# Kernel optimization log

Measured on AMD Instinct MI355X. Metric: run time of the kernel, lower is better.

Reference implementation:

```python
import jax, jax.numpy as jnp
import numpy as np


def _floor_alpha(q, size):
    # tfa interpolate_bilinear clamps floor to [0, size-2] and alpha to [0, 1]
    floor = jnp.clip(jnp.floor(q), 0.0, float(size - 2))
    alpha = jnp.clip(q - floor, 0.0, 1.0)
    return floor.astype(jnp.int32), alpha


def setup_inputs() -> dict:
    key = jax.random.key(0)
    k1, k2 = jax.random.split(key)
    B, H, W, C = 4, 512, 512, 64
    x = jax.random.normal(k1, (B, H, W, C), dtype=jnp.float32)
    flow = jax.random.normal(k2, (B, H, W, 2), dtype=jnp.float32)
    return {"x": x, "flow": flow}


def reference(x, flow):
    B, H, W, C = x.shape
    # meshgrid with indexing='xy': x_grid varies along W, y_grid along H
    xg = jnp.arange(W, dtype=x.dtype)[None, :]          # [1, W]
    yg = jnp.arange(H, dtype=x.dtype)[:, None]          # [H, 1]
    qx = xg + flow[..., 0]                              # [B, H, W]
    qy = yg + flow[..., 1]                              # [B, H, W]

    fy, ay = _floor_alpha(qy, H)                        # int32 [B,H,W], float [B,H,W]
    fx, ax = _floor_alpha(qx, W)

    b = jnp.arange(B, dtype=jnp.int32)[:, None, None]   # [B,1,1] broadcast batch index
    top_left = x[b, fy, fx]                             # [B,H,W,C]
    top_right = x[b, fy, fx + 1]
    bottom_left = x[b, fy + 1, fx]
    bottom_right = x[b, fy + 1, fx + 1]

    ax = ax[..., None]
    ay = ay[..., None]
    interp_top = ax * (top_right - top_left) + top_left
    interp_bottom = ax * (bottom_right - bottom_left) + bottom_left
    return ay * (interp_bottom - interp_top) + interp_top
```

## Files before the change

### kernel.cpp

```cpp
#include <hip/hip_runtime.h>


typedef float f32x4 __attribute__((ext_vector_type(4)));
typedef float f32x2 __attribute__((ext_vector_type(2)));

constexpr int BD = 4;
constexpr int HD = 512;
constexpr int WD = 512;
constexpr int CD = 64;
constexpr int NBLOCKS = BD * HD * WD * 16 / 256;
constexpr int NXCD = 8;
constexpr int CHUNK = NBLOCKS / NXCD;

__global__ __launch_bounds__(256) void warp_bilinear_kernel(
    const float* __restrict__ x,
    const float* __restrict__ flow,
    float* __restrict__ out)
{
    const int bid = (blockIdx.x % NXCD) * CHUNK + (blockIdx.x / NXCD);

    const int gtid = bid * 256 + threadIdx.x;
    const int p    = gtid >> 4;
    const int lane = gtid & 15;
    const int c4   = lane << 2;

    const int w  = p & (WD - 1);
    const int hb = p >> 9;
    const int h  = hb & (HD - 1);
    const int b  = hb >> 9;

    const f32x2 fl =
        __builtin_nontemporal_load(reinterpret_cast<const f32x2*>(flow) + p);
    const float qx = (float)w + fl.x;
    const float qy = (float)h + fl.y;

    float fxf = fminf(fmaxf(floorf(qx), 0.0f), (float)(WD - 2));
    float fyf = fminf(fmaxf(floorf(qy), 0.0f), (float)(HD - 2));
    const float ax = fminf(fmaxf(qx - fxf, 0.0f), 1.0f);
    const float ay = fminf(fmaxf(qy - fyf, 0.0f), 1.0f);
    const int fx = (int)fxf;
    const int fy = (int)fyf;

    const size_t base_idx = ((((size_t)b * HD + fy) * WD + fx) * CD) + c4;
    const float* base = x + base_idx;

    const f32x4 tl = *reinterpret_cast<const f32x4*>(base);
    const f32x4 tr = *reinterpret_cast<const f32x4*>(base + CD);
    const f32x4 bl = *reinterpret_cast<const f32x4*>(base + (size_t)WD * CD);
    const f32x4 br = *reinterpret_cast<const f32x4*>(base + (size_t)WD * CD + CD);

    f32x4 it = (tr - tl) * ax + tl;
    f32x4 ib = (br - bl) * ax + bl;
    f32x4 o  = (ib - it) * ay + it;

    __builtin_nontemporal_store(
        o, reinterpret_cast<f32x4*>(out) + (size_t)p * 16 + lane);
}

extern "C" void kernel_launch(void* const* d_in, const int* in_sizes, int n_in,
                              void* d_out, int out_size, void* d_ws, size_t ws_size,
                              hipStream_t stream) {
    const float* x    = (const float*)d_in[0];
    const float* flow = (const float*)d_in[1];
    float* out        = (float*)d_out;

    warp_bilinear_kernel<<<NBLOCKS, 256, 0, stream>>>(x, flow, out);
}
```

Measured before the change: 99.85 us.

## Process two pixels per thread with eight threads per pixel

Reworks the thread mapping so each thread handles two pixels and eight threads share a pixel, with each thread loading two 16-byte chunks per corner. This cuts the thread count by four and raises the number of loads in flight per thread, to hide gather latency better. Indexing now uses 32-bit ints, which is enough for this problem size. The per-thread accesses inside a pixel become strided by 32 floats, which could change coalescing.

```diff
diff --git a/kernel.cpp b/kernel.cpp
--- a/kernel.cpp
+++ b/kernel.cpp
@@ -8,7 +8,8 @@
 constexpr int HD = 512;
 constexpr int WD = 512;
 constexpr int CD = 64;
-constexpr int NBLOCKS = BD * HD * WD * 16 / 256;
+constexpr int PXB = 64;
+constexpr int NBLOCKS = BD * HD * WD / PXB;
 constexpr int NXCD = 8;
 constexpr int CHUNK = NBLOCKS / NXCD;
 
@@ -17,44 +18,91 @@
     const float* __restrict__ flow,
     float* __restrict__ out)
 {
-    const int bid = (blockIdx.x % NXCD) * CHUNK + (blockIdx.x / NXCD);
+    const int bid = (blockIdx.x & (NXCD - 1)) * CHUNK + (blockIdx.x >> 3);
 
-    const int gtid = bid * 256 + threadIdx.x;
-    const int p    = gtid >> 4;
-    const int lane = gtid & 15;
-    const int c4   = lane << 2;
+    const int pbase = bid * PXB;
+    const int pg  = threadIdx.x >> 3;
+    const int sub = threadIdx.x & 7;
+    const int c0  = sub << 2;
 
-    const int w  = p & (WD - 1);
-    const int hb = p >> 9;
-    const int h  = hb & (HD - 1);
-    const int b  = hb >> 9;
+    const int p0 = pbase + pg;
+    const int p1 = p0 + 32;
 
-    const f32x2 fl =
-        __builtin_nontemporal_load(reinterpret_cast<const f32x2*>(flow) + p);
-    const float qx = (float)w + fl.x;
-    const float qy = (float)h + fl.y;
+    const int row = p0 >> 9;
+    const int h   = row & (HD - 1);
+    const int b   = row >> 9;
+    const float hf = (float)h;
+    const int w0  = p0 & (WD - 1);
+    const int xb  = b * (HD * WD * CD) + c0;
 
-    float fxf = fminf(fmaxf(floorf(qx), 0.0f), (float)(WD - 2));
-    float fyf = fminf(fmaxf(floorf(qy), 0.0f), (float)(HD - 2));
-    const float ax = fminf(fmaxf(qx - fxf, 0.0f), 1.0f);
-    const float ay = fminf(fmaxf(qy - fyf, 0.0f), 1.0f);
-    const int fx = (int)fxf;
-    const int fy = (int)fyf;
+    const f32x2 fl0 =
+        __builtin_nontemporal_load(reinterpret_cast<const f32x2*>(flow) + p0);
+    const f32x2 fl1 =
+        __builtin_nontemporal_load(reinterpret_cast<const f32x2*>(flow) + p1);
 
-    const size_t base_idx = ((((size_t)b * HD + fy) * WD + fx) * CD) + c4;
-    const float* base = x + base_idx;
+    float ax0, ay0, ax1, ay1;
+    int i0, i1;
+    {
+        const float qx = (float)w0 + fl0.x;
+        const float qy = hf + fl0.y;
+        const float fxf = fminf(fmaxf(floorf(qx), 0.0f), (float)(WD - 2));
+        const float fyf = fminf(fmaxf(floorf(qy), 0.0f), (float)(HD - 2));
+        ax0 = fminf(fmaxf(qx - fxf, 0.0f), 1.0f);
+        ay0 = fminf(fmaxf(qy - fyf, 0.0f), 1.0f);
+        i0 = xb + ((int)fyf * WD + (int)fxf) * CD;
+    }
+    {
+        const float qx = (float)(w0 + 32) + fl1.x;
+        const float qy = hf + fl1.y;
+        const float fxf = fminf(fmaxf(floorf(qx), 0.0f), (float)(WD - 2));
+        const float fyf = fminf(fmaxf(floorf(qy), 0.0f), (float)(HD - 2));
+        ax1 = fminf(fmaxf(qx - fxf, 0.0f), 1.0f);
+        ay1 = fminf(fmaxf(qy - fyf, 0.0f), 1.0f);
+        i1 = xb + ((int)fyf * WD + (int)fxf) * CD;
+    }
 
-    const f32x4 tl = *reinterpret_cast<const f32x4*>(base);
-    const f32x4 tr = *reinterpret_cast<const f32x4*>(base + CD);
-    const f32x4 bl = *reinterpret_cast<const f32x4*>(base + (size_t)WD * CD);
-    const f32x4 br = *reinterpret_cast<const f32x4*>(base + (size_t)WD * CD + CD);
+    const float* t0 = x + i0;
+    const float* b0 = t0 + WD * CD;
+    const float* t1 = x + i1;
+    const float* b1 = t1 + WD * CD;
 
-    f32x4 it = (tr - tl) * ax + tl;
-    f32x4 ib = (br - bl) * ax + bl;
-    f32x4 o  = (ib - it) * ay + it;
+    const f32x4 tl0a = *reinterpret_cast<const f32x4*>(t0);
+    const f32x4 tl0b = *reinterpret_cast<const f32x4*>(t0 + 32);
+    const f32x4 tr0a = *reinterpret_cast<const f32x4*>(t0 + CD);
+    const f32x4 tr0b = *reinterpret_cast<const f32x4*>(t0 + CD + 32);
+    const f32x4 bl0a = *reinterpret_cast<const f32x4*>(b0);
+    const f32x4 bl0b = *reinterpret_cast<const f32x4*>(b0 + 32);
+    const f32x4 br0a = *reinterpret_cast<const f32x4*>(b0 + CD);
+    const f32x4 br0b = *reinterpret_cast<const f32x4*>(b0 + CD + 32);
+    const f32x4 tl1a = *reinterpret_cast<const f32x4*>(t1);
+    const f32x4 tl1b = *reinterpret_cast<const f32x4*>(t1 + 32);
+    const f32x4 tr1a = *reinterpret_cast<const f32x4*>(t1 + CD);
+    const f32x4 tr1b = *reinterpret_cast<const f32x4*>(t1 + CD + 32);
+    const f32x4 bl1a = *reinterpret_cast<const f32x4*>(b1);
+    const f32x4 bl1b = *reinterpret_cast<const f32x4*>(b1 + 32);
+    const f32x4 br1a = *reinterpret_cast<const f32x4*>(b1 + CD);
+    const f32x4 br1b = *reinterpret_cast<const f32x4*>(b1 + CD + 32);
 
-    __builtin_nontemporal_store(
-        o, reinterpret_cast<f32x4*>(out) + (size_t)p * 16 + lane);
+    f32x4 it, ib, o0a, o0b, o1a, o1b;
+    it = (tr0a - tl0a) * ax0 + tl0a;
+    ib = (br0a - bl0a) * ax0 + bl0a;
+    o0a = (ib - it) * ay0 + it;
+    it = (tr0b - tl0b) * ax0 + tl0b;
+    ib = (br0b - bl0b) * ax0 + bl0b;
+    o0b = (ib - it) * ay0 + it;
+    it = (tr1a - tl1a) * ax1 + tl1a;
+    ib = (br1a - bl1a) * ax1 + bl1a;
+    o1a = (ib - it) * ay1 + it;
+    it = (tr1b - tl1b) * ax1 + tl1b;
+    ib = (br1b - bl1b) * ax1 + bl1b;
+    o1b = (ib - it) * ay1 + it;
+
+    f32x4* op0 = reinterpret_cast<f32x4*>(out + p0 * CD + c0);
+    f32x4* op1 = reinterpret_cast<f32x4*>(out + p1 * CD + c0);
+    __builtin_nontemporal_store(o0a, op0);
+    __builtin_nontemporal_store(o0b, op0 + 8);
+    __builtin_nontemporal_store(o1a, op1);
+    __builtin_nontemporal_store(o1b, op1 + 8);
 }
 
 extern "C" void kernel_launch(void* const* d_in, const int* in_sizes, int n_in,
```

Measured after the change: 100.6 us. No clear change (+0.8%).
